# Performance work log

Hardware: AMD Instinct MI355X
Metric: run time of the kernel (lower is better)

## Reference

```python
import jax, jax.numpy as jnp
import numpy as np

N_NODES = 50000      # query nodes
NUM_SAMPLE = 25      # sampled neighbors per node
FEAT_DIM = 128
TABLE_SIZE = 100000  # embedding table rows


def setup_inputs() -> dict:
    key = jax.random.key(0)
    k1, k2, k3, k4 = jax.random.split(key, 4)
    neighbors = jax.random.randint(k1, (N_NODES, NUM_SAMPLE), 0, TABLE_SIZE, dtype=jnp.int64)
    emb_table = jax.random.normal(k2, (TABLE_SIZE, FEAT_DIM), dtype=jnp.float32)
    W = jax.random.normal(k3, (FEAT_DIM, FEAT_DIM), dtype=jnp.float32) * (1.0 / np.sqrt(FEAT_DIM))
    b = jax.random.normal(k4, (FEAT_DIM,), dtype=jnp.float32) * 0.01
    return {"neighbors": neighbors, "emb_table": emb_table, "W": W, "b": b}


def reference(neighbors, emb_table, W, b):
    # gather: [n, s, d]
    e = emb_table[neighbors]
    # Linear(feat_dim, feat_dim) + ReLU (torch Linear: x @ W.T + b)
    h = jax.nn.relu(jnp.einsum("nsd,fd->nsf", e, W) + b)
    # mean pool over sampled neighbors -> [n, d]
    return jnp.mean(h, axis=1)
```

## Files before the change

kernel.cpp:

```cpp
#include <hip/hip_runtime.h>
#include <hip/hip_bf16.h>

#define NNODES 50000
#define NSAMP  25
#define FEAT   128
#define TABROWS 100000

typedef __attribute__((ext_vector_type(4))) float  f32x4;
typedef __attribute__((ext_vector_type(2))) float  f32x2;
typedef __attribute__((ext_vector_type(8))) __bf16 bf16x8;

__device__ __forceinline__ bf16x8 cvt2(const f32x4 lo, const f32x4 hi) {
  bf16x8 r;
  r[0] = (__bf16)lo[0]; r[1] = (__bf16)lo[1];
  r[2] = (__bf16)lo[2]; r[3] = (__bf16)lo[3];
  r[4] = (__bf16)hi[0]; r[5] = (__bf16)hi[1];
  r[6] = (__bf16)hi[2]; r[7] = (__bf16)hi[3];
  return r;
}

__global__ __launch_bounds__(256)
void cvt_table_kernel(const float* __restrict__ src, __bf16* __restrict__ dst, int n8)
{
  int i = blockIdx.x * blockDim.x + threadIdx.x;
  const int stride = gridDim.x * blockDim.x;
  for (; i < n8; i += stride) {
    f32x4 lo = ((const f32x4*)src)[2 * i];
    f32x4 hi = ((const f32x4*)src)[2 * i + 1];
    ((bf16x8*)dst)[i] = cvt2(lo, hi);
  }
}

template<int BF16TAB>
__global__ __launch_bounds__(256, 4)
void meanpool_mfma_kernel(const int* __restrict__ nbr,
                          const float* __restrict__ embf32,
                          const __bf16* __restrict__ embbf,
                          const float* __restrict__ W,
                          const float* __restrict__ b,
                          float* __restrict__ out)
{
  __shared__ bf16x8 Blds[8 * 4 * 64];
  __shared__ float  Ot[4][128];

  const int tid  = threadIdx.x;
  const int lane = tid & 63;
  const int wib  = tid >> 6;
  const int wid  = blockIdx.x * 4 + wib;
  const int nWaves = gridDim.x * 4;

  const int col  = lane & 15;
  const int quad = lane >> 4;
  const int coff = quad * 8;

  for (int c = tid; c < 2048; c += 256) {
    const int nt = c >> 8;
    const int kk = (c >> 6) & 3;
    const int l  = c & 63;
    const int f  = nt * 16 + (l & 15);
    const int d0 = kk * 32 + (l >> 4) * 8;
    f32x4 lo = *(const f32x4*)(W + f * FEAT + d0);
    f32x4 hi = *(const f32x4*)(W + f * FEAT + d0 + 4);
    Blds[c] = cvt2(lo, hi);
  }

  float bias[8];
  #pragma unroll
  for (int nt = 0; nt < 8; ++nt) bias[nt] = b[nt * 16 + col];

  __syncthreads();

  const float inv = 1.0f / (float)NSAMP;
  const bool  v1 = (16 + col) < NSAMP;
  const f32x4 zero4 = {0.f, 0.f, 0.f, 0.f};
  const bf16x8 zero8 = {};
  float* osc = &Ot[wib][0];

  for (int n = wid; n < NNODES; n += nWaves) {
    const int* nb = nbr + n * NSAMP;
    const int i0 = nb[col];
    const int i1 = v1 ? nb[16 + col] : 0;

    bf16x8 A0[4], A1[4];
    if (BF16TAB) {
      const __bf16* r0 = embbf + (long long)i0 * FEAT;
      const __bf16* r1 = embbf + (long long)i1 * FEAT;
      #pragma unroll
      for (int kk = 0; kk < 4; ++kk) {
        A0[kk] = *(const bf16x8*)(r0 + kk * 32 + coff);
        A1[kk] = v1 ? *(const bf16x8*)(r1 + kk * 32 + coff) : zero8;
      }
    } else {
      const float* r0 = embf32 + (long long)i0 * FEAT;
      const float* r1 = embf32 + (long long)i1 * FEAT;
      #pragma unroll
      for (int kk = 0; kk < 4; ++kk) {
        f32x4 lo0 = *(const f32x4*)(r0 + kk * 32 + coff);
        f32x4 hi0 = *(const f32x4*)(r0 + kk * 32 + coff + 4);
        A0[kk] = cvt2(lo0, hi0);
        f32x4 lo1 = zero4, hi1 = zero4;
        if (v1) {
          lo1 = *(const f32x4*)(r1 + kk * 32 + coff);
          hi1 = *(const f32x4*)(r1 + kk * 32 + coff + 4);
        }
        A1[kk] = cvt2(lo1, hi1);
      }
    }

    #pragma unroll
    for (int nt = 0; nt < 8; ++nt) {
      f32x4 acc0 = {0.f, 0.f, 0.f, 0.f};
      f32x4 acc1 = {0.f, 0.f, 0.f, 0.f};
      #pragma unroll
      for (int kk = 0; kk < 4; ++kk) {
        const bf16x8 Bf = Blds[nt * 256 + kk * 64 + lane];
        acc0 = __builtin_amdgcn_mfma_f32_16x16x32_bf16(A0[kk], Bf, acc0, 0, 0, 0);
        acc1 = __builtin_amdgcn_mfma_f32_16x16x32_bf16(A1[kk], Bf, acc1, 0, 0, 0);
      }
      float psum = 0.f;
      #pragma unroll
      for (int j = 0; j < 4; ++j) {
        psum += fmaxf(acc0[j] + bias[nt], 0.f);
        const int srow = 16 + quad * 4 + j;
        if (srow < NSAMP) psum += fmaxf(acc1[j] + bias[nt], 0.f);
      }
      psum += __shfl_xor(psum, 16);
      psum += __shfl_xor(psum, 32);
      if (lane < 16) osc[nt * 16 + lane] = psum * inv;
    }
    asm volatile("s_waitcnt lgkmcnt(0)" ::: "memory");
    const f32x2 o2 = *(const f32x2*)(osc + 2 * lane);
    *(f32x2*)(out + (long long)n * FEAT + 2 * lane) = o2;
  }
}

extern "C" void kernel_launch(void* const* d_in, const int* in_sizes, int n_in,
                              void* d_out, int out_size, void* d_ws, size_t ws_size,
                              hipStream_t stream) {
  const int*   nbr = (const int*)d_in[0];
  const float* emb = (const float*)d_in[1];
  const float* W   = (const float*)d_in[2];
  const float* b   = (const float*)d_in[3];
  float* out = (float*)d_out;

  const size_t tabBytes = (size_t)TABROWS * FEAT * sizeof(__bf16);
  const bool useBf16 = ws_size >= tabBytes;

  if (useBf16) {
    __bf16* tab = (__bf16*)d_ws;
    const int n8 = TABROWS * FEAT / 8;
    hipLaunchKernelGGL(cvt_table_kernel, dim3(2048), dim3(256), 0, stream,
                       emb, tab, n8);
    hipLaunchKernelGGL((meanpool_mfma_kernel<1>), dim3(2048), dim3(256), 0, stream,
                       nbr, emb, tab, W, b, out);
  } else {
    hipLaunchKernelGGL((meanpool_mfma_kernel<0>), dim3(2048), dim3(256), 0, stream,
                       nbr, emb, (const __bf16*)nullptr, W, b, out);
  }
}
```

Before: 169.7 us.

## Software-pipeline neighbor row gathers with double-buffered registers across nodes

Restructures the per-wave node loop into a two-stage software pipeline: the embedding rows for the next node are issued and the indices two nodes ahead are loaded before the MFMA compute of the current node, using two sets of register fragments. This aims to hide gather latency behind matrix work. It also drops the per-row sample-validity check in the epilogue and instead subtracts a precomputed correction of 7*relu(bias) for the zero-padded rows. The cost is higher register pressure under launch_bounds(256,4), which may cause spills or reduce occupancy.

```diff
diff --git a/kernel.cpp b/kernel.cpp
--- a/kernel.cpp
+++ b/kernel.cpp
@@ -47,7 +47,7 @@
   const int lane = tid & 63;
   const int wib  = tid >> 6;
   const int wid  = blockIdx.x * 4 + wib;
-  const int nWaves = gridDim.x * 4;
+  const int nW   = gridDim.x * 4;
 
   const int col  = lane & 15;
   const int quad = lane >> 4;
@@ -64,24 +64,27 @@
     Blds[c] = cvt2(lo, hi);
   }
 
-  float bias[8];
+  float bias[8], bcor[8];
   #pragma unroll
-  for (int nt = 0; nt < 8; ++nt) bias[nt] = b[nt * 16 + col];
+  for (int nt = 0; nt < 8; ++nt) {
+    bias[nt] = b[nt * 16 + col];
+    bcor[nt] = 7.0f * fmaxf(bias[nt], 0.f);
+  }
 
   __syncthreads();
 
   const float inv = 1.0f / (float)NSAMP;
   const bool  v1 = (16 + col) < NSAMP;
-  const f32x4 zero4 = {0.f, 0.f, 0.f, 0.f};
   const bf16x8 zero8 = {};
   float* osc = &Ot[wib][0];
 
-  for (int n = wid; n < NNODES; n += nWaves) {
+  auto load_idx = [&](int n, int& i0, int& i1) {
     const int* nb = nbr + n * NSAMP;
-    const int i0 = nb[col];
-    const int i1 = v1 ? nb[16 + col] : 0;
+    i0 = nb[col];
+    i1 = v1 ? nb[16 + col] : 0;
+  };
 
-    bf16x8 A0[4], A1[4];
+  auto issue_rows = [&](int i0, int i1, bf16x8* A0, bf16x8* A1) {
     if (BF16TAB) {
       const __bf16* r0 = embbf + (long long)i0 * FEAT;
       const __bf16* r1 = embbf + (long long)i1 * FEAT;
@@ -98,7 +101,8 @@
         f32x4 lo0 = *(const f32x4*)(r0 + kk * 32 + coff);
         f32x4 hi0 = *(const f32x4*)(r0 + kk * 32 + coff + 4);
         A0[kk] = cvt2(lo0, hi0);
-        f32x4 lo1 = zero4, hi1 = zero4;
+        f32x4 z = {0.f, 0.f, 0.f, 0.f};
+        f32x4 lo1 = z, hi1 = z;
         if (v1) {
           lo1 = *(const f32x4*)(r1 + kk * 32 + coff);
           hi1 = *(const f32x4*)(r1 + kk * 32 + coff + 4);
@@ -106,7 +110,9 @@
         A1[kk] = cvt2(lo1, hi1);
       }
     }
+  };
 
+  auto compute_node = [&](const bf16x8* A0, const bf16x8* A1, int n) {
     #pragma unroll
     for (int nt = 0; nt < 8; ++nt) {
       f32x4 acc0 = {0.f, 0.f, 0.f, 0.f};
@@ -121,16 +127,41 @@
       #pragma unroll
       for (int j = 0; j < 4; ++j) {
         psum += fmaxf(acc0[j] + bias[nt], 0.f);
-        const int srow = 16 + quad * 4 + j;
-        if (srow < NSAMP) psum += fmaxf(acc1[j] + bias[nt], 0.f);
+        psum += fmaxf(acc1[j] + bias[nt], 0.f);
       }
       psum += __shfl_xor(psum, 16);
       psum += __shfl_xor(psum, 32);
-      if (lane < 16) osc[nt * 16 + lane] = psum * inv;
+      if (lane < 16) osc[nt * 16 + lane] = (psum - bcor[nt]) * inv;
     }
     asm volatile("s_waitcnt lgkmcnt(0)" ::: "memory");
     const f32x2 o2 = *(const f32x2*)(osc + 2 * lane);
     *(f32x2*)(out + (long long)n * FEAT + 2 * lane) = o2;
+  };
+
+  bf16x8 Aa0[4], Aa1[4], Ab0[4], Ab1[4];
+  int i0b = 0, i1b = 0;
+
+  {
+    int i0a, i1a;
+    load_idx(wid, i0a, i1a);
+    issue_rows(i0a, i1a, Aa0, Aa1);
+    if (wid + nW < NNODES) load_idx(wid + nW, i0b, i1b);
+  }
+
+  for (int n = wid; n < NNODES; n += 2 * nW) {
+    const int n1 = n + nW, n2 = n + 2 * nW, n3 = n + 3 * nW;
+
+    if (n1 < NNODES) issue_rows(i0b, i1b, Ab0, Ab1);
+    int i0c = 0, i1c = 0;
+    if (n2 < NNODES) load_idx(n2, i0c, i1c);
+    compute_node(Aa0, Aa1, n);
+
+    if (n2 < NNODES) issue_rows(i0c, i1c, Aa0, Aa1);
+    int i0d = 0, i1d = 0;
+    if (n3 < NNODES) load_idx(n3, i0d, i1d);
+    if (n1 < NNODES) compute_node(Ab0, Ab1, n1);
+
+    i0b = i0d; i1b = i1d;
   }
 }
 
```

Result: no change. 172.8 us (+1.8%).

## Process two nodes per wave to reuse LDS weight fragments and widen stores

Applied to the files above, without the earlier changes.

Each wave now handles a pair of nodes, issuing four MFMA chains per weight fragment read from LDS instead of two. This halves LDS reads of W per node and adds independent MFMA work for latency hiding. The bias is folded into the accumulator init and the padded-row masking is replaced by subtracting a constant correction for the 7 zero rows. Output stores become 16-byte vectors covering two rows. The cost is higher register pressure from four A fragment sets, which could reduce occupancy under the launch bounds.

```diff
diff --git a/kernel.cpp b/kernel.cpp
--- a/kernel.cpp
+++ b/kernel.cpp
@@ -1,13 +1,13 @@
 #include <hip/hip_runtime.h>
 #include <hip/hip_bf16.h>
 
-#define NNODES 50000
-#define NSAMP  25
-#define FEAT   128
+#define NNODES  50000
+#define NPAIRS  25000
+#define NSAMP   25
+#define FEAT    128
 #define TABROWS 100000
 
 typedef __attribute__((ext_vector_type(4))) float  f32x4;
-typedef __attribute__((ext_vector_type(2))) float  f32x2;
 typedef __attribute__((ext_vector_type(8))) __bf16 bf16x8;
 
 __device__ __forceinline__ bf16x8 cvt2(const f32x4 lo, const f32x4 hi) {
@@ -41,13 +41,13 @@
                           float* __restrict__ out)
 {
   __shared__ bf16x8 Blds[8 * 4 * 64];
-  __shared__ float  Ot[4][128];
+  __shared__ float  Ot[4][256];
 
   const int tid  = threadIdx.x;
   const int lane = tid & 63;
   const int wib  = tid >> 6;
   const int wid  = blockIdx.x * 4 + wib;
-  const int nWaves = gridDim.x * 4;
+  const int nW   = gridDim.x * 4;
 
   const int col  = lane & 15;
   const int quad = lane >> 4;
@@ -71,66 +71,77 @@
   __syncthreads();
 
   const float inv = 1.0f / (float)NSAMP;
-  const bool  v1 = (16 + col) < NSAMP;
-  const f32x4 zero4 = {0.f, 0.f, 0.f, 0.f};
+  const bool  v1 = col < 9;
   const bf16x8 zero8 = {};
   float* osc = &Ot[wib][0];
 
-  for (int n = wid; n < NNODES; n += nWaves) {
-    const int* nb = nbr + n * NSAMP;
-    const int i0 = nb[col];
-    const int i1 = v1 ? nb[16 + col] : 0;
+  for (int p = wid; p < NPAIRS; p += nW) {
+    const int n0 = 2 * p;
+    const int* nbA = nbr + (long long)n0 * NSAMP;
+    const int* nbB = nbA + NSAMP;
+    const int ia0 = nbA[col];
+    const int ia1 = v1 ? nbA[16 + col] : 0;
+    const int ib0 = nbB[col];
+    const int ib1 = v1 ? nbB[16 + col] : 0;
 
-    bf16x8 A0[4], A1[4];
+    bf16x8 Aa0[4], Aa1[4], Ab0[4], Ab1[4];
     if (BF16TAB) {
-      const __bf16* r0 = embbf + (long long)i0 * FEAT;
-      const __bf16* r1 = embbf + (long long)i1 * FEAT;
+      const __bf16* ra0 = embbf + (long long)ia0 * FEAT + coff;
+      const __bf16* ra1 = embbf + (long long)ia1 * FEAT + coff;
+      const __bf16* rb0 = embbf + (long long)ib0 * FEAT + coff;
+      const __bf16* rb1 = embbf + (long long)ib1 * FEAT + coff;
       #pragma unroll
       for (int kk = 0; kk < 4; ++kk) {
-        A0[kk] = *(const bf16x8*)(r0 + kk * 32 + coff);
-        A1[kk] = v1 ? *(const bf16x8*)(r1 + kk * 32 + coff) : zero8;
+        Aa0[kk] = *(const bf16x8*)(ra0 + kk * 32);
+        Aa1[kk] = v1 ? *(const bf16x8*)(ra1 + kk * 32) : zero8;
+        Ab0[kk] = *(const bf16x8*)(rb0 + kk * 32);
+        Ab1[kk] = v1 ? *(const bf16x8*)(rb1 + kk * 32) : zero8;
       }
     } else {
-      const float* r0 = embf32 + (long long)i0 * FEAT;
-      const float* r1 = embf32 + (long long)i1 * FEAT;
+      const float* ra0 = embf32 + (long long)ia0 * FEAT + coff;
+      const float* ra1 = embf32 + (long long)ia1 * FEAT + coff;
+      const float* rb0 = embf32 + (long long)ib0 * FEAT + coff;
+      const float* rb1 = embf32 + (long long)ib1 * FEAT + coff;
+      const f32x4 z = {0.f, 0.f, 0.f, 0.f};
       #pragma unroll
       for (int kk = 0; kk < 4; ++kk) {
-        f32x4 lo0 = *(const f32x4*)(r0 + kk * 32 + coff);
-        f32x4 hi0 = *(const f32x4*)(r0 + kk * 32 + coff + 4);
-        A0[kk] = cvt2(lo0, hi0);
-        f32x4 lo1 = zero4, hi1 = zero4;
-        if (v1) {
-          lo1 = *(const f32x4*)(r1 + kk * 32 + coff);
-          hi1 = *(const f32x4*)(r1 + kk * 32 + coff + 4);
-        }
-        A1[kk] = cvt2(lo1, hi1);
+        Aa0[kk] = cvt2(*(const f32x4*)(ra0 + kk * 32), *(const f32x4*)(ra0 + kk * 32 + 4));
+        Aa1[kk] = v1 ? cvt2(*(const f32x4*)(ra1 + kk * 32), *(const f32x4*)(ra1 + kk * 32 + 4)) : cvt2(z, z);
+        Ab0[kk] = cvt2(*(const f32x4*)(rb0 + kk * 32), *(const f32x4*)(rb0 + kk * 32 + 4));
+        Ab1[kk] = v1 ? cvt2(*(const f32x4*)(rb1 + kk * 32), *(const f32x4*)(rb1 + kk * 32 + 4)) : cvt2(z, z);
       }
     }
 
     #pragma unroll
     for (int nt = 0; nt < 8; ++nt) {
-      f32x4 acc0 = {0.f, 0.f, 0.f, 0.f};
-      f32x4 acc1 = {0.f, 0.f, 0.f, 0.f};
+      const float bn = bias[nt];
+      f32x4 acc0a = {bn, bn, bn, bn};
+      f32x4 acc1a = {bn, bn, bn, bn};
+      f32x4 acc0b = {bn, bn, bn, bn};
+      f32x4 acc1b = {bn, bn, bn, bn};
       #pragma unroll
       for (int kk = 0; kk < 4; ++kk) {
         const bf16x8 Bf = Blds[nt * 256 + kk * 64 + lane];
-        acc0 = __builtin_amdgcn_mfma_f32_16x16x32_bf16(A0[kk], Bf, acc0, 0, 0, 0);
-        acc1 = __builtin_amdgcn_mfma_f32_16x16x32_bf16(A1[kk], Bf, acc1, 0, 0, 0);
+        acc0a = __builtin_amdgcn_mfma_f32_16x16x32_bf16(Aa0[kk], Bf, acc0a, 0, 0, 0);
+        acc1a = __builtin_amdgcn_mfma_f32_16x16x32_bf16(Aa1[kk], Bf, acc1a, 0, 0, 0);
+        acc0b = __builtin_amdgcn_mfma_f32_16x16x32_bf16(Ab0[kk], Bf, acc0b, 0, 0, 0);
+        acc1b = __builtin_amdgcn_mfma_f32_16x16x32_bf16(Ab1[kk], Bf, acc1b, 0, 0, 0);
       }
-      float psum = 0.f;
+      float psA = 0.f, psB = 0.f;
       #pragma unroll
       for (int j = 0; j < 4; ++j) {
-        psum += fmaxf(acc0[j] + bias[nt], 0.f);
-        const int srow = 16 + quad * 4 + j;
-        if (srow < NSAMP) psum += fmaxf(acc1[j] + bias[nt], 0.f);
+        psA += fmaxf(acc0a[j], 0.f) + fmaxf(acc1a[j], 0.f);
+        psB += fmaxf(acc0b[j], 0.f) + fmaxf(acc1b[j], 0.f);
       }
-      psum += __shfl_xor(psum, 16);
-      psum += __shfl_xor(psum, 32);
-      if (lane < 16) osc[nt * 16 + lane] = psum * inv;
+      psA += __shfl_xor(psA, 16);  psA += __shfl_xor(psA, 32);
+      psB += __shfl_xor(psB, 16);  psB += __shfl_xor(psB, 32);
+      const float corr = 7.0f * fmaxf(bias[nt], 0.f);
+      if (quad == 0) osc[nt * 16 + col]       = (psA - corr) * inv;
+      if (quad == 1) osc[128 + nt * 16 + col] = (psB - corr) * inv;
     }
     asm volatile("s_waitcnt lgkmcnt(0)" ::: "memory");
-    const f32x2 o2 = *(const f32x2*)(osc + 2 * lane);
-    *(f32x2*)(out + (long long)n * FEAT + 2 * lane) = o2;
+    const f32x4 o4 = *(const f32x4*)(osc + 4 * lane);
+    *(f32x4*)(out + (long long)n0 * FEAT + 4 * lane) = o4;
   }
 }
 
```

After: 197.9 us. +16.6%, slower.
